# Kernel tuning notes

Hardware: AMD Instinct MI355X
Metric: run time of the kernel (lower is better)

## Reference

```python
import jax, jax.numpy as jnp
import numpy as np

N_SEQ, N_TOK, C_M, C, C_Z = 512, 384, 64, 32, 128


def setup_inputs() -> dict:
    key = jax.random.key(0)
    k1, k2, k3, k4 = jax.random.split(key, 4)
    scale = 1.0 / np.sqrt(C_M)
    return {
        "msa_feat": jax.random.normal(k1, (N_SEQ, N_TOK, C_M), dtype=jnp.float32),
        "msa_mask": jnp.ones((N_SEQ, N_TOK), dtype=jnp.float32),
        "gamma": jnp.ones((C_M,), dtype=jnp.float32),
        "beta": jnp.zeros((C_M,), dtype=jnp.float32),
        "Wa": jax.random.normal(k2, (C_M, C), dtype=jnp.float32) * scale,
        "Wb": jax.random.normal(k3, (C_M, C), dtype=jnp.float32) * scale,
        "Wout": jax.random.normal(k4, (C * C, C_Z), dtype=jnp.float32) * (1.0 / C),
        "bout": jnp.zeros((C_Z,), dtype=jnp.float32),
    }


def reference(msa_feat, msa_mask, gamma, beta, Wa, Wb, Wout, bout):
    # LayerNorm over c_m (eps matches torch default 1e-5)
    mu = jnp.mean(msa_feat, axis=-1, keepdims=True)
    var = jnp.mean(jnp.square(msa_feat - mu), axis=-1, keepdims=True)
    m = (msa_feat - mu) * jax.lax.rsqrt(var + 1e-5) * gamma + beta

    mask = msa_mask[..., None]                       # [s, i, 1]
    a = (m @ Wa) * mask                              # [s, i, c]
    b = (m @ Wb) * mask                              # [s, j, c]

    # Outer product contracted over MSA rows s: [i, j, c, c]
    ab = jnp.einsum('sic,sjd->ijcd', a, b)
    n_tok = a.shape[-2]
    ab = ab.reshape(n_tok, n_tok, C * C)             # [i, j, c*c]

    z = ab @ Wout + bout                             # [i, j, c_z]
    norm = jnp.einsum('si,sj->ij', msa_mask, msa_mask)
    return z / (norm[..., None] + 0.001)
```

## Files before the change

kernel.cpp:

```cpp
#include <hip/hip_runtime.h>
#include <cstdint>
#include <cstddef>

#define NS 512
#define NT 384
#define CZ 128

typedef __bf16 bf16x8 __attribute__((ext_vector_type(8)));
typedef __bf16 bf16x4 __attribute__((ext_vector_type(4)));
typedef float floatx16 __attribute__((ext_vector_type(16)));


__global__ __launch_bounds__(256) void prep_wout(const float* __restrict__ Wout,
                                                 __bf16* __restrict__ WT) {
  const int idx = blockIdx.x * 256 + threadIdx.x;
  const int e = idx >> 10, kk = idx & 1023;
  const int round = kk >> 9, rem = kk & 511, d = rem >> 4, cp = rem & 15;
  const int c = round * 16 + cp;
  WT[idx] = (__bf16)Wout[(size_t)(c * 32 + d) * CZ + e];
}

__global__ __launch_bounds__(256) void prep_norm(const float* __restrict__ mask,
                                                 float* __restrict__ rnorm) {
  __shared__ float mi[512];
  const int i = blockIdx.x, t = threadIdx.x;
  mi[t]       = mask[(size_t)t * NT + i];
  mi[t + 256] = mask[(size_t)(t + 256) * NT + i];
  __syncthreads();
  for (int j = t; j < NT; j += 256) {
    float acc = 0.f;
#pragma unroll 4
    for (int s = 0; s < NS; ++s) acc += mi[s] * mask[(size_t)s * NT + j];
    rnorm[(size_t)i * NT + j] = 1.0f / (acc + 0.001f);
  }
}

__global__ __launch_bounds__(64) void ln_proj(const float* __restrict__ feat,
                                              const float* __restrict__ mask,
                                              const float* __restrict__ gamma,
                                              const float* __restrict__ beta,
                                              const float* __restrict__ Wa,
                                              const float* __restrict__ Wb,
                                              __bf16* __restrict__ Abf,
                                              __bf16* __restrict__ Bbf) {
  __shared__ float tile[64][65];
  __shared__ __bf16 T[32 * 72];
  const int bid = blockIdx.x;
  const int i = bid >> 3;
  const int s0 = (bid & 7) << 6;
  const int lane = threadIdx.x;
  const int l31 = lane & 31, lh = lane >> 5;

  const int rsub = lane >> 4, cb = (lane & 15) * 4;
#pragma unroll
  for (int rr = 0; rr < 16; ++rr) {
    const int row = rr * 4 + rsub;
    const float4 v = *(const float4*)(feat + ((size_t)(s0 + row) * NT + i) * 64 + cb);
    tile[row][cb] = v.x; tile[row][cb + 1] = v.y;
    tile[row][cb + 2] = v.z; tile[row][cb + 3] = v.w;
  }
  __syncthreads();

  float x[64];
#pragma unroll
  for (int k = 0; k < 64; ++k) x[k] = tile[lane][k];

  float mu = 0.f;
#pragma unroll
  for (int k = 0; k < 64; ++k) mu += x[k];
  mu *= (1.0f / 64.0f);
  float var = 0.f;
#pragma unroll
  for (int k = 0; k < 64; ++k) { const float d = x[k] - mu; var += d * d; }
  var *= (1.0f / 64.0f);
  const float rstd = rsqrtf(var + 1e-5f);
#pragma unroll
  for (int k = 0; k < 64; ++k)
    x[k] = (x[k] - mu) * rstd * gamma[k] + beta[k];

  const float mv = mask[(size_t)(s0 + lane) * NT + i];

  float acc[32];
#pragma unroll
  for (int c = 0; c < 32; ++c) acc[c] = 0.f;
#pragma unroll 8
  for (int k = 0; k < 64; ++k) {
    const float mk = x[k];
#pragma unroll
    for (int c = 0; c < 32; ++c) acc[c] = fmaf(mk, Wa[k * 32 + c], acc[c]);
  }
#pragma unroll
  for (int c = 0; c < 32; ++c) T[c * 72 + lane] = (__bf16)(acc[c] * mv);
  __syncthreads();
  {
    __bf16* dst = Abf + (size_t)(i >> 2) * 65536 + (size_t)(s0 >> 3) * 1024 +
                  (size_t)((i & 3) * 32) * 8;
#pragma unroll
    for (int q = 0; q < 4; ++q) {
      const bf16x8 v = *(const bf16x8*)(T + l31 * 72 + (q * 2 + lh) * 8);
      *(bf16x8*)(dst + (size_t)(q * 2 + lh) * 1024 + l31 * 8) = v;
    }
  }
  __syncthreads();

#pragma unroll
  for (int c = 0; c < 32; ++c) acc[c] = 0.f;
#pragma unroll 8
  for (int k = 0; k < 64; ++k) {
    const float mk = x[k];
#pragma unroll
    for (int c = 0; c < 32; ++c) acc[c] = fmaf(mk, Wb[k * 32 + c], acc[c]);
  }
#pragma unroll
  for (int c = 0; c < 32; ++c) T[c * 72 + lane] = (__bf16)(acc[c] * mv);
  __syncthreads();
  {
    __bf16* dst = Bbf + (size_t)(i >> 3) * 131072 + (size_t)(s0 >> 3) * 2048 +
                  (size_t)((i & 7) * 32) * 8;
#pragma unroll
    for (int q = 0; q < 4; ++q) {
      const bf16x8 v = *(const bf16x8*)(T + l31 * 72 + (q * 2 + lh) * 8);
      *(bf16x8*)(dst + (size_t)(q * 2 + lh) * 2048 + l31 * 8) = v;
    }
  }
}

__global__ __launch_bounds__(256) void opm_gemm(const __bf16* __restrict__ A,
                                                const __bf16* __restrict__ B,
                                                const __bf16* __restrict__ WT,
                                                const float* __restrict__ bout,
                                                const float* __restrict__ rnorm,
                                                float* __restrict__ out) {
  __shared__ __align__(16) __bf16 smem[24576];

  const int t = threadIdx.x, lane = t & 63, wid = t >> 6;
  const int wm = wid & 1, wn = wid >> 1;
  const int l31 = lane & 31, lh = lane >> 5;
  const int bm = blockIdx.x % 96, bn = blockIdx.x / 96;

  const __bf16* Apan = A + (size_t)bm * 65536;
  const __bf16* Bpan = B + (size_t)bn * 131072;

  floatx16 acc[2][4];
#pragma unroll
  for (int fm = 0; fm < 2; ++fm)
#pragma unroll
    for (int fn = 0; fn < 4; ++fn)
#pragma unroll
      for (int q = 0; q < 16; ++q) acc[fm][fn][q] = 0.f;

#define STAGE(kt, buf)                                                          \
  {                                                                             \
    __bf16* dst = smem + (buf) * 12288;                                         \
    _Pragma("unroll")                                                           \
    for (int g2 = 0; g2 < 2; ++g2) {                                            \
      const int g = wid * 2 + g2;                                               \
      __builtin_amdgcn_global_load_lds(                                         \
          (const __attribute__((address_space(1))) void*)(Apan + (kt) * 4096 +  \
                                                          g * 512 + lane * 8),  \
          (__attribute__((address_space(3))) void*)(dst + g * 512), 16, 0, 0);  \
    }                                                                           \
    _Pragma("unroll")                                                           \
    for (int g4 = 0; g4 < 4; ++g4) {                                            \
      const int g = wid * 4 + g4;                                               \
      __builtin_amdgcn_global_load_lds(                                         \
          (const __attribute__((address_space(1))) void*)(Bpan + (kt) * 8192 +  \
                                                          g * 512 + lane * 8),  \
          (__attribute__((address_space(3))) void*)(dst + 4096 + g * 512),      \
          16, 0, 0);                                                            \
    }                                                                           \
  }

  STAGE(0, 0);
  int buf = 0;
  for (int kt = 0; kt < 16; ++kt) {
    __syncthreads();
    if (kt < 15) STAGE(kt + 1, buf ^ 1);
    const __bf16* As = smem + buf * 12288;
    const __bf16* Bs = As + 4096;
#pragma unroll
    for (int ks = 0; ks < 2; ++ks) {
      const int ck = ks * 2 + lh;
      bf16x8 af[2], bf[4];
#pragma unroll
      for (int fm = 0; fm < 2; ++fm)
        af[fm] = *(const bf16x8*)(As + ck * 1024 + (wm * 64 + fm * 32 + l31) * 8);
#pragma unroll
      for (int fn = 0; fn < 4; ++fn)
        bf[fn] = *(const bf16x8*)(Bs + ck * 2048 + (wn * 128 + fn * 32 + l31) * 8);
#pragma unroll
      for (int fm = 0; fm < 2; ++fm)
#pragma unroll
        for (int fn = 0; fn < 4; ++fn)
          acc[fm][fn] = __builtin_amdgcn_mfma_f32_32x32x16_bf16(af[fm], bf[fn],
                                                                acc[fm][fn], 0, 0, 0);
    }
    buf ^= 1;
  }
#undef STAGE

  floatx16 z;
#pragma unroll
  for (int q = 0; q < 16; ++q) z[q] = 0.f;
  const int e = wid * 32 + l31;

#pragma unroll
  for (int round = 0; round < 2; ++round) {
    __syncthreads();
#pragma unroll
    for (int fm = 0; fm < 2; ++fm)
#pragma unroll
      for (int fn = 0; fn < 4; ++fn) {
        const int p = (wm * 2 + fm) * 8 + wn * 4 + fn;
        __bf16* base = smem + p * 648 + l31 * 20 + lh * 4;
#pragma unroll
        for (int qp = 0; qp < 2; ++qp) {
          bf16x4 v;
#pragma unroll
          for (int j = 0; j < 4; ++j)
            v[j] = (__bf16)acc[fm][fn][round * 8 + qp * 4 + j];
          *(bf16x4*)(base + qp * 8) = v;
        }
      }
    __syncthreads();
    const __bf16* wrow = WT + (size_t)e * 1024 + round * 512 + lh * 8;
    const __bf16* prow = smem + l31 * 648 + lh * 8;
#pragma unroll 8
    for (int ks = 0; ks < 32; ++ks) {
      const bf16x8 pa = *(const bf16x8*)(prow + ks * 20);
      const bf16x8 wb = *(const bf16x8*)(wrow + ks * 16);
      z = __builtin_amdgcn_mfma_f32_32x32x16_bf16(pa, wb, z, 0, 0, 0);
    }
  }

  const float be = bout[e];
#pragma unroll
  for (int r = 0; r < 16; ++r) {
    const int p = (r & 3) + 8 * (r >> 2) + 4 * lh;
    const int i = bm * 4 + (p >> 3), j = bn * 8 + (p & 7);
    const float rn = rnorm[(size_t)i * NT + j];
    out[((size_t)i * NT + j) * CZ + e] = (z[r] + be) * rn;
  }
}

extern "C" void kernel_launch(void* const* d_in, const int* in_sizes, int n_in,
                              void* d_out, int out_size, void* d_ws, size_t ws_size,
                              hipStream_t stream) {
  const float* feat  = (const float*)d_in[0];
  const float* mask  = (const float*)d_in[1];
  const float* gamma = (const float*)d_in[2];
  const float* beta  = (const float*)d_in[3];
  const float* Wa    = (const float*)d_in[4];
  const float* Wb    = (const float*)d_in[5];
  const float* Wout  = (const float*)d_in[6];
  const float* bout  = (const float*)d_in[7];
  float* out = (float*)d_out;

  char* ws = (char*)d_ws;
  const size_t AB_BYTES = (size_t)96 * 65536 * sizeof(__bf16);
  __bf16* Abf = (__bf16*)(ws);
  __bf16* Bbf = (__bf16*)(ws + AB_BYTES);
  __bf16* WT  = (__bf16*)(ws + 2 * AB_BYTES);
  float* rnorm = (float*)(ws + 2 * AB_BYTES + (size_t)CZ * 1024 * sizeof(__bf16));

  prep_wout<<<512, 256, 0, stream>>>(Wout, WT);
  prep_norm<<<NT, 256, 0, stream>>>(mask, rnorm);
  ln_proj<<<NT * (NS / 64), 64, 0, stream>>>(feat, mask, gamma, beta, Wa, Wb, Abf, Bbf);
  opm_gemm<<<96 * 48, 256, 0, stream>>>(Abf, Bbf, WT, bout, rnorm, out);
}
```

Measured before the change: 447.2 us.

## Triple-buffer OPM GEMM with vmcnt waits, XCD block swizzle, and LDS reuse in ln_proj

```diff
diff --git a/kernel.cpp b/kernel.cpp
--- a/kernel.cpp
+++ b/kernel.cpp
@@ -43,8 +43,8 @@
                                               const float* __restrict__ Wb,
                                               __bf16* __restrict__ Abf,
                                               __bf16* __restrict__ Bbf) {
-  __shared__ float tile[64][65];
-  __shared__ __bf16 T[32 * 72];
+  __shared__ __align__(16) float ubuf[64 * 65];
+  __bf16* T = (__bf16*)ubuf;
   const int bid = blockIdx.x;
   const int i = bid >> 3;
   const int s0 = (bid & 7) << 6;
@@ -56,14 +56,14 @@
   for (int rr = 0; rr < 16; ++rr) {
     const int row = rr * 4 + rsub;
     const float4 v = *(const float4*)(feat + ((size_t)(s0 + row) * NT + i) * 64 + cb);
-    tile[row][cb] = v.x; tile[row][cb + 1] = v.y;
-    tile[row][cb + 2] = v.z; tile[row][cb + 3] = v.w;
+    ubuf[row * 65 + cb] = v.x; ubuf[row * 65 + cb + 1] = v.y;
+    ubuf[row * 65 + cb + 2] = v.z; ubuf[row * 65 + cb + 3] = v.w;
   }
   __syncthreads();
 
   float x[64];
 #pragma unroll
-  for (int k = 0; k < 64; ++k) x[k] = tile[lane][k];
+  for (int k = 0; k < 64; ++k) x[k] = ubuf[lane * 65 + k];
 
   float mu = 0.f;
 #pragma unroll
@@ -89,6 +89,7 @@
 #pragma unroll
     for (int c = 0; c < 32; ++c) acc[c] = fmaf(mk, Wa[k * 32 + c], acc[c]);
   }
+  __syncthreads();
 #pragma unroll
   for (int c = 0; c < 32; ++c) T[c * 72 + lane] = (__bf16)(acc[c] * mv);
   __syncthreads();
@@ -131,12 +132,13 @@
                                                 const float* __restrict__ bout,
                                                 const float* __restrict__ rnorm,
                                                 float* __restrict__ out) {
-  __shared__ __align__(16) __bf16 smem[24576];
+  __shared__ __align__(16) __bf16 smem[36864];
 
   const int t = threadIdx.x, lane = t & 63, wid = t >> 6;
   const int wm = wid & 1, wn = wid >> 1;
   const int l31 = lane & 31, lh = lane >> 5;
-  const int bm = blockIdx.x % 96, bn = blockIdx.x / 96;
+  const int bid = (blockIdx.x & 7) * 576 + (blockIdx.x >> 3);
+  const int bm = bid % 96, bn = bid / 96;
 
   const __bf16* Apan = A + (size_t)bm * 65536;
   const __bf16* Bpan = B + (size_t)bn * 131072;
@@ -149,55 +151,79 @@
 #pragma unroll
       for (int q = 0; q < 16; ++q) acc[fm][fn][q] = 0.f;
 
-#define STAGE(kt, buf)                                                          \
+#define STAGE(kt, OFF)                                                          \
   {                                                                             \
-    __bf16* dst = smem + (buf) * 12288;                                         \
+    __bf16* dst = smem + (OFF);                                                 \
     _Pragma("unroll")                                                           \
     for (int g2 = 0; g2 < 2; ++g2) {                                            \
       const int g = wid * 2 + g2;                                               \
       __builtin_amdgcn_global_load_lds(                                         \
-          (const __attribute__((address_space(1))) void*)(Apan + (kt) * 4096 +  \
-                                                          g * 512 + lane * 8),  \
+          (const __attribute__((address_space(1))) void*)(Apan +                \
+              (size_t)(kt) * 4096 + g * 512 + lane * 8),                        \
           (__attribute__((address_space(3))) void*)(dst + g * 512), 16, 0, 0);  \
     }                                                                           \
     _Pragma("unroll")                                                           \
     for (int g4 = 0; g4 < 4; ++g4) {                                            \
       const int g = wid * 4 + g4;                                               \
       __builtin_amdgcn_global_load_lds(                                         \
-          (const __attribute__((address_space(1))) void*)(Bpan + (kt) * 8192 +  \
-                                                          g * 512 + lane * 8),  \
+          (const __attribute__((address_space(1))) void*)(Bpan +                \
+              (size_t)(kt) * 8192 + g * 512 + lane * 8),                        \
           (__attribute__((address_space(3))) void*)(dst + 4096 + g * 512),      \
           16, 0, 0);                                                            \
     }                                                                           \
   }
 
+#define COMPUTE(OFF)                                                            \
+  {                                                                             \
+    const __bf16* As = smem + (OFF);                                            \
+    const __bf16* Bs = As + 4096;                                               \
+    __builtin_amdgcn_s_setprio(1);                                              \
+    _Pragma("unroll")                                                           \
+    for (int ks = 0; ks < 2; ++ks) {                                            \
+      const int ck = ks * 2 + lh;                                               \
+      bf16x8 af[2], bfv[4];                                                     \
+      _Pragma("unroll")                                                         \
+      for (int fm = 0; fm < 2; ++fm)                                            \
+        af[fm] = *(const bf16x8*)(As + ck * 1024 + (wm * 64 + fm * 32 + l31) * 8); \
+      _Pragma("unroll")                                                         \
+      for (int fn = 0; fn < 4; ++fn)                                            \
+        bfv[fn] = *(const bf16x8*)(Bs + ck * 2048 + (wn * 128 + fn * 32 + l31) * 8); \
+      _Pragma("unroll")                                                         \
+      for (int fm = 0; fm < 2; ++fm)                                            \
+        _Pragma("unroll")                                                       \
+        for (int fn = 0; fn < 4; ++fn)                                          \
+          acc[fm][fn] = __builtin_amdgcn_mfma_f32_32x32x16_bf16(                \
+              af[fm], bfv[fn], acc[fm][fn], 0, 0, 0);                           \
+    }                                                                           \
+    __builtin_amdgcn_s_setprio(0);                                              \
+  }
+
   STAGE(0, 0);
-  int buf = 0;
-  for (int kt = 0; kt < 16; ++kt) {
-    __syncthreads();
-    if (kt < 15) STAGE(kt + 1, buf ^ 1);
-    const __bf16* As = smem + buf * 12288;
-    const __bf16* Bs = As + 4096;
-#pragma unroll
-    for (int ks = 0; ks < 2; ++ks) {
-      const int ck = ks * 2 + lh;
-      bf16x8 af[2], bf[4];
-#pragma unroll
-      for (int fm = 0; fm < 2; ++fm)
-        af[fm] = *(const bf16x8*)(As + ck * 1024 + (wm * 64 + fm * 32 + l31) * 8);
-#pragma unroll
-      for (int fn = 0; fn < 4; ++fn)
-        bf[fn] = *(const bf16x8*)(Bs + ck * 2048 + (wn * 128 + fn * 32 + l31) * 8);
-#pragma unroll
-      for (int fm = 0; fm < 2; ++fm)
-#pragma unroll
-        for (int fn = 0; fn < 4; ++fn)
-          acc[fm][fn] = __builtin_amdgcn_mfma_f32_32x32x16_bf16(af[fm], bf[fn],
-                                                                acc[fm][fn], 0, 0, 0);
-    }
-    buf ^= 1;
-  }
+  STAGE(1, 12288);
+
+  unsigned o0 = 0, o1 = 12288, o2 = 24576;
+  for (int kt = 0; kt < 14; ++kt) {
+    asm volatile("s_waitcnt vmcnt(6)");
+    STAGE(kt + 2, o2);
+    __builtin_amdgcn_s_barrier();
+    __builtin_amdgcn_sched_barrier(0);
+    COMPUTE(o0);
+    __builtin_amdgcn_s_barrier();
+    const unsigned tmp = o0; o0 = o1; o1 = o2; o2 = tmp;
+  }
+  asm volatile("s_waitcnt vmcnt(6)");
+  __builtin_amdgcn_s_barrier();
+  __builtin_amdgcn_sched_barrier(0);
+  COMPUTE(o0);
+  __builtin_amdgcn_s_barrier();
+  { const unsigned tmp = o0; o0 = o1; o1 = o2; o2 = tmp; }
+  asm volatile("s_waitcnt vmcnt(0)");
+  __builtin_amdgcn_s_barrier();
+  __builtin_amdgcn_sched_barrier(0);
+  COMPUTE(o0);
+  __builtin_amdgcn_s_barrier();
 #undef STAGE
+#undef COMPUTE
 
   floatx16 z;
 #pragma unroll
```

Measured after the change: 436.5 us. 2.4% less time.

## Halve OPM GEMM tile to 4x4 token pairs with 16x16 MFMA projection

Applied to the files above, without the earlier changes.

```diff
diff --git a/kernel.cpp b/kernel.cpp
--- a/kernel.cpp
+++ b/kernel.cpp
@@ -9,6 +9,7 @@
 typedef __bf16 bf16x8 __attribute__((ext_vector_type(8)));
 typedef __bf16 bf16x4 __attribute__((ext_vector_type(4)));
 typedef float floatx16 __attribute__((ext_vector_type(16)));
+typedef float floatx4 __attribute__((ext_vector_type(4)));
 
 
 __global__ __launch_bounds__(256) void prep_wout(const float* __restrict__ Wout,
@@ -43,8 +44,8 @@
                                               const float* __restrict__ Wb,
                                               __bf16* __restrict__ Abf,
                                               __bf16* __restrict__ Bbf) {
-  __shared__ float tile[64][65];
-  __shared__ __bf16 T[32 * 72];
+  __shared__ __align__(16) float ubuf[64 * 65];
+  __bf16* T = (__bf16*)ubuf;
   const int bid = blockIdx.x;
   const int i = bid >> 3;
   const int s0 = (bid & 7) << 6;
@@ -56,14 +57,14 @@
   for (int rr = 0; rr < 16; ++rr) {
     const int row = rr * 4 + rsub;
     const float4 v = *(const float4*)(feat + ((size_t)(s0 + row) * NT + i) * 64 + cb);
-    tile[row][cb] = v.x; tile[row][cb + 1] = v.y;
-    tile[row][cb + 2] = v.z; tile[row][cb + 3] = v.w;
+    ubuf[row * 65 + cb] = v.x; ubuf[row * 65 + cb + 1] = v.y;
+    ubuf[row * 65 + cb + 2] = v.z; ubuf[row * 65 + cb + 3] = v.w;
   }
   __syncthreads();
 
   float x[64];
 #pragma unroll
-  for (int k = 0; k < 64; ++k) x[k] = tile[lane][k];
+  for (int k = 0; k < 64; ++k) x[k] = ubuf[lane * 65 + k];
 
   float mu = 0.f;
 #pragma unroll
@@ -89,6 +90,7 @@
 #pragma unroll
     for (int c = 0; c < 32; ++c) acc[c] = fmaf(mk, Wa[k * 32 + c], acc[c]);
   }
+  __syncthreads();
 #pragma unroll
   for (int c = 0; c < 32; ++c) T[c * 72 + lane] = (__bf16)(acc[c] * mv);
   __syncthreads();
@@ -125,47 +127,49 @@
   }
 }
 
-__global__ __launch_bounds__(256) void opm_gemm(const __bf16* __restrict__ A,
-                                                const __bf16* __restrict__ B,
-                                                const __bf16* __restrict__ WT,
-                                                const float* __restrict__ bout,
-                                                const float* __restrict__ rnorm,
-                                                float* __restrict__ out) {
-  __shared__ __align__(16) __bf16 smem[24576];
+__global__ __launch_bounds__(256, 4) void opm_gemm(const __bf16* __restrict__ A,
+                                                   const __bf16* __restrict__ B,
+                                                   const __bf16* __restrict__ WT,
+                                                   const float* __restrict__ bout,
+                                                   const float* __restrict__ rnorm,
+                                                   float* __restrict__ out) {
+  __shared__ __align__(16) __bf16 smem[16384];
 
   const int t = threadIdx.x, lane = t & 63, wid = t >> 6;
   const int wm = wid & 1, wn = wid >> 1;
   const int l31 = lane & 31, lh = lane >> 5;
+  const int l15 = lane & 15, lq = lane >> 4;
   const int bm = blockIdx.x % 96, bn = blockIdx.x / 96;
 
   const __bf16* Apan = A + (size_t)bm * 65536;
-  const __bf16* Bpan = B + (size_t)bn * 131072;
-
-  floatx16 acc[2][4];
+  const __bf16* Bpan = B + (size_t)(bn >> 1) * 131072 + (size_t)(bn & 1) * 1024;
+
+  floatx16 acc[2][2];
 #pragma unroll
   for (int fm = 0; fm < 2; ++fm)
 #pragma unroll
-    for (int fn = 0; fn < 4; ++fn)
+    for (int fn = 0; fn < 2; ++fn)
 #pragma unroll
       for (int q = 0; q < 16; ++q) acc[fm][fn][q] = 0.f;
 
-#define STAGE(kt, buf)                                                          \
+#define STAGE(kt, OFF)                                                          \
   {                                                                             \
-    __bf16* dst = smem + (buf) * 12288;                                         \
+    __bf16* dst = smem + (OFF);                                                 \
     _Pragma("unroll")                                                           \
     for (int g2 = 0; g2 < 2; ++g2) {                                            \
       const int g = wid * 2 + g2;                                               \
       __builtin_amdgcn_global_load_lds(                                         \
-          (const __attribute__((address_space(1))) void*)(Apan + (kt) * 4096 +  \
-                                                          g * 512 + lane * 8),  \
+          (const __attribute__((address_space(1))) void*)(Apan +                \
+              (size_t)(kt) * 4096 + g * 512 + lane * 8),                        \
           (__attribute__((address_space(3))) void*)(dst + g * 512), 16, 0, 0);  \
     }                                                                           \
     _Pragma("unroll")                                                           \
-    for (int g4 = 0; g4 < 4; ++g4) {                                            \
-      const int g = wid * 4 + g4;                                               \
+    for (int g2 = 0; g2 < 2; ++g2) {                                            \
+      const int g = wid * 2 + g2;                          \
       __builtin_amdgcn_global_load_lds(                                         \
-          (const __attribute__((address_space(1))) void*)(Bpan + (kt) * 8192 +  \
-                                                          g * 512 + lane * 8),  \
+          (const __attribute__((address_space(1))) void*)(Bpan +                \
+              (size_t)((kt) * 4 + (g >> 1)) * 2048 + (g & 1) * 512 +            \
+              lane * 8),                                                        \
           (__attribute__((address_space(3))) void*)(dst + 4096 + g * 512),      \
           16, 0, 0);                                                            \
     }                                                                           \
@@ -175,34 +179,38 @@
   int buf = 0;
   for (int kt = 0; kt < 16; ++kt) {
     __syncthreads();
-    if (kt < 15) STAGE(kt + 1, buf ^ 1);
-    const __bf16* As = smem + buf * 12288;
+    if (kt < 15) STAGE(kt + 1, buf ^ 1 ? 8192 : 0);
+    const __bf16* As = smem + (buf ? 8192 : 0);
     const __bf16* Bs = As + 4096;
+    __builtin_amdgcn_s_setprio(1);
 #pragma unroll
     for (int ks = 0; ks < 2; ++ks) {
       const int ck = ks * 2 + lh;
-      bf16x8 af[2], bf[4];
+      bf16x8 af[2], bfv[2];
 #pragma unroll
       for (int fm = 0; fm < 2; ++fm)
         af[fm] = *(const bf16x8*)(As + ck * 1024 + (wm * 64 + fm * 32 + l31) * 8);
 #pragma unroll
-      for (int fn = 0; fn < 4; ++fn)
-        bf[fn] = *(const bf16x8*)(Bs + ck * 2048 + (wn * 128 + fn * 32 + l31) * 8);
+      for (int fn = 0; fn < 2; ++fn)
+        bfv[fn] = *(const bf16x8*)(Bs + ck * 1024 + (wn * 64 + fn * 32 + l31) * 8);
 #pragma unroll
       for (int fm = 0; fm < 2; ++fm)
 #pragma unroll
-        for (int fn = 0; fn < 4; ++fn)
-          acc[fm][fn] = __builtin_amdgcn_mfma_f32_32x32x16_bf16(af[fm], bf[fn],
+        for (int fn = 0; fn < 2; ++fn)
+          acc[fm][fn] = __builtin_amdgcn_mfma_f32_32x32x16_bf16(af[fm], bfv[fn],
                                                                 acc[fm][fn], 0, 0, 0);
     }
+    __builtin_amdgcn_s_setprio(0);
     buf ^= 1;
   }
 #undef STAGE
 
-  floatx16 z;
-#pragma unroll
-  for (int q = 0; q < 16; ++q) z[q] = 0.f;
-  const int e = wid * 32 + l31;
+  floatx4 zf[2];
+#pragma unroll
+  for (int ef = 0; ef < 2; ++ef)
+#pragma unroll
+    for (int q = 0; q < 4; ++q) zf[ef][q] = 0.f;
+  const int e0 = wid * 32;
 
 #pragma unroll
   for (int round = 0; round < 2; ++round) {
@@ -210,9 +218,9 @@
 #pragma unroll
     for (int fm = 0; fm < 2; ++fm)
 #pragma unroll
-      for (int fn = 0; fn < 4; ++fn) {
-        const int p = (wm * 2 + fm) * 8 + wn * 4 + fn;
-        __bf16* base = smem + p * 648 + l31 * 20 + lh * 4;
+      for (int fn = 0; fn < 2; ++fn) {
+        const int p = (wm * 2 + fm) * 4 + (wn * 2 + fn);
+        __bf16* base = smem + p * 516 + l31 * 16 + lh * 4;
 #pragma unroll
         for (int qp = 0; qp < 2; ++qp) {
           bf16x4 v;
@@ -223,23 +231,30 @@
         }
       }
     __syncthreads();
-    const __bf16* wrow = WT + (size_t)e * 1024 + round * 512 + lh * 8;
-    const __bf16* prow = smem + l31 * 648 + lh * 8;
-#pragma unroll 8
-    for (int ks = 0; ks < 32; ++ks) {
-      const bf16x8 pa = *(const bf16x8*)(prow + ks * 20);
-      const bf16x8 wb = *(const bf16x8*)(wrow + ks * 16);
-      z = __builtin_amdgcn_mfma_f32_32x32x16_bf16(pa, wb, z, 0, 0, 0);
-    }
-  }
-
-  const float be = bout[e];
-#pragma unroll
-  for (int r = 0; r < 16; ++r) {
-    const int p = (r & 3) + 8 * (r >> 2) + 4 * lh;
-    const int i = bm * 4 + (p >> 3), j = bn * 8 + (p & 7);
-    const float rn = rnorm[(size_t)i * NT + j];
-    out[((size_t)i * NT + j) * CZ + e] = (z[r] + be) * rn;
+    const __bf16* prow = smem + l15 * 516 + lq * 8;
+    const __bf16* wrow0 = WT + (size_t)(e0 + l15) * 1024 + round * 512 + lq * 8;
+    const __bf16* wrow1 = wrow0 + (size_t)16 * 1024;
+#pragma unroll 4
+    for (int ks = 0; ks < 16; ++ks) {
+      const bf16x8 pa = *(const bf16x8*)(prow + ks * 32);
+      const bf16x8 wb0 = *(const bf16x8*)(wrow0 + ks * 32);
+      const bf16x8 wb1 = *(const bf16x8*)(wrow1 + ks * 32);
+      zf[0] = __builtin_amdgcn_mfma_f32_16x16x32_bf16(pa, wb0, zf[0], 0, 0, 0);
+      zf[1] = __builtin_amdgcn_mfma_f32_16x16x32_bf16(pa, wb1, zf[1], 0, 0, 0);
+    }
+  }
+
+#pragma unroll
+  for (int ef = 0; ef < 2; ++ef) {
+    const int e = e0 + ef * 16 + l15;
+    const float be = bout[e];
+#pragma unroll
+    for (int q = 0; q < 4; ++q) {
+      const int p = lq * 4 + q;
+      const int i = bm * 4 + (p >> 2), j = bn * 4 + (p & 3);
+      const float rn = rnorm[(size_t)i * NT + j];
+      out[((size_t)i * NT + j) * CZ + e] = (zf[ef][q] + be) * rn;
+    }
   }
 }
 
@@ -266,5 +281,5 @@
   prep_wout<<<512, 256, 0, stream>>>(Wout, WT);
   prep_norm<<<NT, 256, 0, stream>>>(mask, rnorm);
   ln_proj<<<NT * (NS / 64), 64, 0, stream>>>(feat, mask, gamma, beta, Wa, Wb, Abf, Bbf);
-  opm_gemm<<<96 * 48, 256, 0, stream>>>(Abf, Bbf, WT, bout, rnorm, out);
-}
+  opm_gemm<<<96 * 96, 256, 0, stream>>>(Abf, Bbf, WT, bout, rnorm, out);
+}
```

New measurement: 549.3 us. 22.8% more time.
